# Kernel tuning notes

Measured on AMD Instinct MI355X. Metric: run time of the kernel, lower is better.

The kernel has to match this reference:

```python
import jax, jax.numpy as jnp
import numpy as np

D_X, D_K, D_V = 1024, 128, 128
B, N = 8, 2048


def setup_inputs() -> dict:
    key = jax.random.key(0)
    ks = jax.random.split(key, 7)
    s = lambda fan_in: 1.0 / np.sqrt(fan_in)
    return {
        "x": jax.random.normal(ks[0], (B, N, D_X), dtype=jnp.float32),
        "w_q": jax.random.uniform(ks[1], (D_K, D_X), jnp.float32, -s(D_X), s(D_X)),
        "b_q": jax.random.uniform(ks[2], (D_K,), jnp.float32, -s(D_X), s(D_X)),
        "w_k": jax.random.uniform(ks[3], (D_K, D_X), jnp.float32, -s(D_X), s(D_X)),
        "b_k": jax.random.uniform(ks[4], (D_K,), jnp.float32, -s(D_X), s(D_X)),
        "w_v": jax.random.uniform(ks[5], (D_V, D_X), jnp.float32, -s(D_X), s(D_X)),
        "b_v": jax.random.uniform(ks[6], (D_V,), jnp.float32, -s(D_X), s(D_X)),
    }


def reference(x, w_q, b_q, w_k, b_k, w_v, b_v):
    # Q is computed in the original module but unused; omit (no effect on output).
    K = jnp.einsum('bnx,kx->bnk', x, w_k) + b_k  # [B,N,d_k]
    V = jnp.einsum('bnx,vx->bnv', x, w_v) + b_v  # [B,N,d_v]
    # logits = K @ V^T / sqrt(d_k)  -> [B,N,N]  (note: K vs V, not Q vs K)
    scale = 1.0 / np.sqrt(D_K).astype(np.float32)
    logits = jnp.einsum('bnk,bmk->bnm', K, V) * scale
    attn = jax.nn.softmax(logits, axis=-1)
    return jnp.einsum('bnm,bmv->bnv', attn, V)
```

## Files before the change

### kernel.cpp

```cpp
#include <hip/hip_runtime.h>
#include <hip/hip_bf16.h>


typedef short s16x8 __attribute__((ext_vector_type(8)));
typedef float f32x4 __attribute__((ext_vector_type(4)));
typedef unsigned short u16;

#define AS1 __attribute__((address_space(1)))
#define AS3 __attribute__((address_space(3)))

__device__ __forceinline__ void gld_lds16(const void* g, void* l) {
  __builtin_amdgcn_global_load_lds((const AS1 unsigned int*)g, (AS3 unsigned int*)l, 16, 0, 0);
}

__device__ __forceinline__ float bf2f(u16 u) {
  unsigned int v = ((unsigned int)u) << 16;
  return __builtin_bit_cast(float, v);
}
__device__ __forceinline__ u16 f2bf(float f) {
  unsigned int u = __builtin_bit_cast(unsigned int, f);
  u += 0x7fffu + ((u >> 16) & 1u);
  return (u16)(u >> 16);
}
__device__ __forceinline__ unsigned pack_bf2(float a, float b) {
  unsigned ua = __builtin_bit_cast(unsigned, a) + 0x8000u;
  unsigned ub = __builtin_bit_cast(unsigned, b) + 0x8000u;
  return __builtin_amdgcn_perm(ub, ua, 0x07060302u);
}

__global__ __launch_bounds__(256, 4) void wconv_kernel(
    const float* __restrict__ wk, const float* __restrict__ wv,
    u16* __restrict__ wbf)
{
  const int e = (blockIdx.x * 256 + threadIdx.x) * 8;
  const float* src = (e < 131072) ? (wk + e) : (wv + (e - 131072));
  float4 a = *(const float4*)src;
  float4 b = *(const float4*)(src + 4);
  union { unsigned u[4]; s16x8 v; } pk;
  pk.u[0] = pack_bf2(a.x, a.y); pk.u[1] = pack_bf2(a.z, a.w);
  pk.u[2] = pack_bf2(b.x, b.y); pk.u[3] = pack_bf2(b.z, b.w);
  *(s16x8*)(wbf + e) = pk.v;
}

__global__ __launch_bounds__(256, 2) void kv_gemm_kernel(
    const float* __restrict__ x, const u16* __restrict__ wbf,
    const float* __restrict__ bk, const float* __restrict__ bv,
    u16* __restrict__ Kout, u16* __restrict__ Vout, u16* __restrict__ VTout)
{
  __shared__ u16 sA[2][4 * 512];
  __shared__ u16 sB[2][32 * 512];

  const int tid  = threadIdx.x;
  const int wave = tid >> 6;
  const int lane = tid & 63;
  const int l16  = lane & 15;
  const int lq   = lane >> 4;
  const int row0 = blockIdx.x * 32;

  f32x4 acc[2][4];
  for (int i = 0; i < 2; ++i)
    for (int j = 0; j < 4; ++j) acc[i][j] = (f32x4){0.f, 0.f, 0.f, 0.f};

  const int kc = tid & 7, arow = tid >> 3;
  const float* aSrc = x + (size_t)(row0 + arow) * 1024 + kc * 8;
  const int aSlot = ((((arow >> 4) * 2 + (kc >> 2)) * 64) + (kc & 3) * 16 + (arow & 15)) * 8;

  const u16* bSrc[8];
  for (int i = 0; i < 8; ++i) {
    const int sl = wave + i * 4;
    bSrc[i] = wbf + (size_t)((sl >> 1) * 16 + l16) * 1024 + (sl & 1) * 32 + lq * 8;
  }

  float4 p0a = *(const float4*)(aSrc);
  float4 p0b = *(const float4*)(aSrc + 4);
  float4 p1a = *(const float4*)(aSrc + 64);
  float4 p1b = *(const float4*)(aSrc + 68);
  for (int i = 0; i < 8; ++i)
    gld_lds16(bSrc[i], &sB[0][(wave + i * 4) * 512]);

  for (int s = 0; s < 16; ++s) {
    const int buf = s & 1;
    {
      union { unsigned u[4]; s16x8 v; } pk;
      pk.u[0] = pack_bf2(p0a.x, p0a.y); pk.u[1] = pack_bf2(p0a.z, p0a.w);
      pk.u[2] = pack_bf2(p0b.x, p0b.y); pk.u[3] = pack_bf2(p0b.z, p0b.w);
      *(s16x8*)(&sA[buf][aSlot]) = pk.v;
    }
    __syncthreads();
    if (s + 1 < 16)
      for (int i = 0; i < 8; ++i)
        gld_lds16(bSrc[i] + (s + 1) * 64, &sB[buf ^ 1][(wave + i * 4) * 512]);
    p0a = p1a; p0b = p1b;
    if (s + 2 < 16) {
      p1a = *(const float4*)(aSrc + (s + 2) * 64);
      p1b = *(const float4*)(aSrc + (s + 2) * 64 + 4);
    }
    s16x8 af[2][2], bf[4][2];
    for (int rb = 0; rb < 2; ++rb)
      for (int ks = 0; ks < 2; ++ks)
        af[rb][ks] = *(const s16x8*)(&sA[buf][((rb * 2 + ks) * 64 + lane) * 8]);
    for (int cb = 0; cb < 4; ++cb)
      for (int ks = 0; ks < 2; ++ks)
        bf[cb][ks] = *(const s16x8*)(&sB[buf][(((wave * 4 + cb) * 2 + ks) * 64 + lane) * 8]);
    for (int rb = 0; rb < 2; ++rb)
      for (int cb = 0; cb < 4; ++cb)
        for (int ks = 0; ks < 2; ++ks)
          acc[rb][cb] = __builtin_amdgcn_mfma_f32_16x16x32_bf16(af[rb][ks], bf[cb][ks], acc[rb][cb], 0, 0, 0);
  }

  const int  colBase = wave * 64;
  const bool isV = (wave >= 2);
  u16* outN = isV ? Vout : Kout;
  float fbias[4];
  for (int cb = 0; cb < 4; ++cb) {
    const int col = colBase + cb * 16 + l16;
    fbias[cb] = isV ? bv[col - 128] : bk[col];
  }
  for (int rb = 0; rb < 2; ++rb) {
    const int grow0 = row0 + rb * 16 + lq * 4;
    for (int cb = 0; cb < 4; ++cb) {
      const int gcol = colBase + cb * 16 + l16;
      const int ocol = isV ? (gcol - 128) : gcol;
      union { u16 u[4]; unsigned long long ull; } pk;
      for (int r = 0; r < 4; ++r) {
        u16 h = f2bf(acc[rb][cb][r] + fbias[cb]);
        outN[(size_t)(grow0 + r) * 128 + ocol] = h;
        pk.u[r] = h;
      }
      if (isV) {
        const int bidx = grow0 >> 11;
        const int n    = grow0 & 2047;
        *(unsigned long long*)(VTout + (size_t)bidx * 128 * 2048 + (size_t)ocol * 2048 + n) = pk.ull;
      }
    }
  }
}

__global__ __launch_bounds__(256, 2) void flash_kernel(
    const u16* __restrict__ Kmat, const u16* __restrict__ Vmat,
    const u16* __restrict__ VT, float* __restrict__ out,
    float* __restrict__ Opart, float* __restrict__ lbuf)
{
  __shared__ u16 sV[2][16 * 512];
  __shared__ u16 sVT[2][16 * 512];
  __shared__ u16 sP[64 * 66];

  const int tid  = threadIdx.x;
  const int wave = tid >> 6;
  const int lane = tid & 63;
  const int l16  = lane & 15;
  const int lq   = lane >> 4;
  const int b    = blockIdx.y;
  const int q0   = blockIdx.x * 64;
  const int z    = blockIdx.z;
  const int ntiles = (2048 / gridDim.z) / 64;
  const int mstart = z * (2048 / gridDim.z);
  const float scale = 0.08838834764831845f;

  s16x8 kf[4];
  {
    const u16* Kb = Kmat + ((size_t)b * 2048 + q0 + wave * 16 + l16) * 128 + lq * 8;
    for (int ks = 0; ks < 4; ++ks) kf[ks] = *(const s16x8*)(Kb + ks * 32);
  }

  const u16* vSrc[4];  const u16* vtSrc[4];
  {
    const u16* Vb  = Vmat + (size_t)b * 2048 * 128;
    const u16* VTb = VT   + (size_t)b * 128 * 2048;
    for (int i = 0; i < 4; ++i) {
      const int sl = wave + i * 4;
      vSrc[i]  = Vb  + (size_t)((sl >> 2) * 16 + l16) * 128 + (sl & 3) * 32 + lq * 8;
      vtSrc[i] = VTb + (size_t)((sl >> 1) * 16 + l16) * 2048 + (sl & 1) * 32 + lq * 8;
    }
  }

  f32x4 oacc[8];
  for (int v = 0; v < 8; ++v) oacc[v] = (f32x4){0.f, 0.f, 0.f, 0.f};
  float lrow[4] = {0.f, 0.f, 0.f, 0.f};

  for (int i = 0; i < 4; ++i) {
    gld_lds16(vSrc[i] + (size_t)mstart * 128, &sV[0][(wave + i * 4) * 512]);
    gld_lds16(vtSrc[i] + mstart,              &sVT[0][(wave + i * 4) * 512]);
  }

  for (int mt = 0; mt < ntiles; ++mt) {
    const int buf = mt & 1;
    __syncthreads();
    if (mt + 1 < ntiles) {
      const int m1 = mstart + (mt + 1) * 64;
      for (int i = 0; i < 4; ++i) {
        gld_lds16(vSrc[i] + (size_t)m1 * 128, &sV[buf ^ 1][(wave + i * 4) * 512]);
        gld_lds16(vtSrc[i] + m1,              &sVT[buf ^ 1][(wave + i * 4) * 512]);
      }
    }

    f32x4 sacc[4];
    for (int t = 0; t < 4; ++t) sacc[t] = (f32x4){0.f, 0.f, 0.f, 0.f};
    for (int ks = 0; ks < 4; ++ks)
      for (int t = 0; t < 4; ++t)
        sacc[t] = __builtin_amdgcn_mfma_f32_16x16x32_bf16(
            kf[ks], *(const s16x8*)(&sV[buf][(t * 4 + ks) * 512 + lane * 8]), sacc[t], 0, 0, 0);

    for (int r = 0; r < 4; ++r) {
      const int prow = (wave * 16 + lq * 4 + r) * 66;
      float rs = 0.f;
      for (int t = 0; t < 4; ++t) {
        float p = __expf(sacc[t][r] * scale);
        u16 h = f2bf(p);
        sP[prow + t * 16 + l16] = h;
        rs += bf2f(h);
      }
      lrow[r] += rs;
    }

    for (int ksm = 0; ksm < 2; ++ksm) {
      s16x8 a = *(const s16x8*)(&sP[(wave * 16 + l16) * 66 + ksm * 32 + lq * 8]);
      for (int v = 0; v < 8; ++v)
        oacc[v] = __builtin_amdgcn_mfma_f32_16x16x32_bf16(
            a, *(const s16x8*)(&sVT[buf][(v * 2 + ksm) * 512 + lane * 8]), oacc[v], 0, 0, 0);
    }
  }

  for (int r = 0; r < 4; ++r) {
    lrow[r] += __shfl_xor(lrow[r], 1);
    lrow[r] += __shfl_xor(lrow[r], 2);
    lrow[r] += __shfl_xor(lrow[r], 4);
    lrow[r] += __shfl_xor(lrow[r], 8);
  }

  const size_t rowg = (size_t)b * 2048 + q0 + wave * 16;
  if (gridDim.z == 1) {
    for (int r = 0; r < 4; ++r) {
      const float inv = 1.f / lrow[r];
      for (int v = 0; v < 8; ++v)
        out[(rowg + lq * 4 + r) * 128 + v * 16 + l16] = oacc[v][r] * inv;
    }
  } else {
    float* Op = Opart + (size_t)z * 2097152;
    float* lp = lbuf + (size_t)z * 32768;
    for (int r = 0; r < 4; ++r)
      for (int v = 0; v < 8; ++v)
        Op[(rowg + lq * 4 + r) * 128 + v * 16 + l16] = oacc[v][r];
    if (l16 == 0)
      for (int r = 0; r < 4; ++r)
        lp[rowg + lq * 4 + r] = lrow[r];
  }
}

__global__ __launch_bounds__(256, 4) void combine_kernel(
    const float* __restrict__ Opart, const float* __restrict__ lbuf,
    float* __restrict__ out)
{
  const int idx = blockIdx.x * 256 + threadIdx.x;
  const int row = idx >> 5;
  const float4 o0 = ((const float4*)Opart)[idx];
  const float4 o1 = ((const float4*)(Opart + 2097152))[idx];
  const float inv = 1.f / (lbuf[row] + lbuf[32768 + row]);
  float4 o;
  o.x = (o0.x + o1.x) * inv;
  o.y = (o0.y + o1.y) * inv;
  o.z = (o0.z + o1.z) * inv;
  o.w = (o0.w + o1.w) * inv;
  ((float4*)out)[idx] = o;
}

extern "C" void kernel_launch(void* const* d_in, const int* in_sizes, int n_in,
                              void* d_out, int out_size, void* d_ws, size_t ws_size,
                              hipStream_t stream) {
  const float* x  = (const float*)d_in[0];
  const float* wk = (const float*)d_in[3];
  const float* bk = (const float*)d_in[4];
  const float* wv = (const float*)d_in[5];
  const float* bv = (const float*)d_in[6];

  u16* ws   = (u16*)d_ws;
  u16* wbf  = ws;
  u16* Kmat = ws + 262144;
  u16* Vmat = Kmat + (size_t)16384 * 128;
  u16* VTm  = Vmat + (size_t)16384 * 128;
  float* Opart = (float*)(VTm + (size_t)16384 * 128);
  float* lbuf  = Opart + 2 * 2097152;
  const bool split = ws_size >= (size_t)30200000;

  wconv_kernel<<<128, 256, 0, stream>>>(wk, wv, wbf);
  kv_gemm_kernel<<<512, 256, 0, stream>>>(x, wbf, bk, bv, Kmat, Vmat, VTm);
  if (split) {
    flash_kernel<<<dim3(32, 8, 2), 256, 0, stream>>>(Kmat, Vmat, VTm,
                                                     (float*)d_out, Opart, lbuf);
    combine_kernel<<<2048, 256, 0, stream>>>(Opart, lbuf, (float*)d_out);
  } else {
    flash_kernel<<<dim3(32, 8, 1), 256, 0, stream>>>(Kmat, Vmat, VTm,
                                                     (float*)d_out, Opart, lbuf);
  }
}
```

Before: 182.0 us.

## Load GEMM weights and V tiles directly into registers instead of LDS staging

```diff
diff --git a/kernel.cpp b/kernel.cpp
--- a/kernel.cpp
+++ b/kernel.cpp
@@ -5,13 +5,6 @@
 typedef short s16x8 __attribute__((ext_vector_type(8)));
 typedef float f32x4 __attribute__((ext_vector_type(4)));
 typedef unsigned short u16;
-
-#define AS1 __attribute__((address_space(1)))
-#define AS3 __attribute__((address_space(3)))
-
-__device__ __forceinline__ void gld_lds16(const void* g, void* l) {
-  __builtin_amdgcn_global_load_lds((const AS1 unsigned int*)g, (AS3 unsigned int*)l, 16, 0, 0);
-}
 
 __device__ __forceinline__ float bf2f(u16 u) {
   unsigned int v = ((unsigned int)u) << 16;
@@ -26,6 +19,9 @@
   unsigned ua = __builtin_bit_cast(unsigned, a) + 0x8000u;
   unsigned ub = __builtin_bit_cast(unsigned, b) + 0x8000u;
   return __builtin_amdgcn_perm(ub, ua, 0x07060302u);
+}
+__device__ __forceinline__ void lgkm_barrier() {
+  asm volatile("s_waitcnt lgkmcnt(0)\n\ts_barrier" ::: "memory");
 }
 
 __global__ __launch_bounds__(256, 4) void wconv_kernel(
@@ -48,7 +44,6 @@
     u16* __restrict__ Kout, u16* __restrict__ Vout, u16* __restrict__ VTout)
 {
   __shared__ u16 sA[2][4 * 512];
-  __shared__ u16 sB[2][32 * 512];
 
   const int tid  = threadIdx.x;
   const int wave = tid >> 6;
@@ -65,47 +60,61 @@
   const float* aSrc = x + (size_t)(row0 + arow) * 1024 + kc * 8;
   const int aSlot = ((((arow >> 4) * 2 + (kc >> 2)) * 64) + (kc & 3) * 16 + (arow & 15)) * 8;
 
-  const u16* bSrc[8];
-  for (int i = 0; i < 8; ++i) {
-    const int sl = wave + i * 4;
-    bSrc[i] = wbf + (size_t)((sl >> 1) * 16 + l16) * 1024 + (sl & 1) * 32 + lq * 8;
-  }
-
-  float4 p0a = *(const float4*)(aSrc);
-  float4 p0b = *(const float4*)(aSrc + 4);
-  float4 p1a = *(const float4*)(aSrc + 64);
-  float4 p1b = *(const float4*)(aSrc + 68);
-  for (int i = 0; i < 8; ++i)
-    gld_lds16(bSrc[i], &sB[0][(wave + i * 4) * 512]);
+  const u16* bBase = wbf + (size_t)(wave * 64 + l16) * 1024 + lq * 8;
+  s16x8 bcur[8], bnxt[8];
+
+  {
+    float4 a0 = *(const float4*)aSrc;
+    float4 a1 = *(const float4*)(aSrc + 4);
+    union { unsigned u[4]; s16x8 v; } pk;
+    pk.u[0] = pack_bf2(a0.x, a0.y); pk.u[1] = pack_bf2(a0.z, a0.w);
+    pk.u[2] = pack_bf2(a1.x, a1.y); pk.u[3] = pack_bf2(a1.z, a1.w);
+    *(s16x8*)(&sA[0][aSlot]) = pk.v;
+  }
+  float4 p0a = *(const float4*)(aSrc + 64);
+  float4 p0b = *(const float4*)(aSrc + 68);
+  float4 p1a, p1b;
+#pragma unroll
+  for (int f = 0; f < 8; ++f)
+    bcur[f] = *(const s16x8*)(bBase + (f >> 1) * 16384 + (f & 1) * 32);
+  lgkm_barrier();
 
   for (int s = 0; s < 16; ++s) {
     const int buf = s & 1;
-    {
+    s16x8 af[2][2];
+#pragma unroll
+    for (int rb = 0; rb < 2; ++rb)
+#pragma unroll
+      for (int ks = 0; ks < 2; ++ks)
+        af[rb][ks] = *(const s16x8*)(&sA[buf][((rb * 2 + ks) * 64 + lane) * 8]);
+    if (s + 1 < 16) {
+      const int koff = (s + 1) * 64;
+#pragma unroll
+      for (int f = 0; f < 8; ++f)
+        bnxt[f] = *(const s16x8*)(bBase + (f >> 1) * 16384 + (f & 1) * 32 + koff);
+    }
+    if (s + 2 < 16) {
+      p1a = *(const float4*)(aSrc + (s + 2) * 64);
+      p1b = *(const float4*)(aSrc + (s + 2) * 64 + 4);
+    }
+#pragma unroll
+    for (int rb = 0; rb < 2; ++rb)
+#pragma unroll
+      for (int cb = 0; cb < 4; ++cb)
+#pragma unroll
+        for (int ks = 0; ks < 2; ++ks)
+          acc[rb][cb] = __builtin_amdgcn_mfma_f32_16x16x32_bf16(
+              af[rb][ks], bcur[cb * 2 + ks], acc[rb][cb], 0, 0, 0);
+    if (s + 1 < 16) {
       union { unsigned u[4]; s16x8 v; } pk;
       pk.u[0] = pack_bf2(p0a.x, p0a.y); pk.u[1] = pack_bf2(p0a.z, p0a.w);
       pk.u[2] = pack_bf2(p0b.x, p0b.y); pk.u[3] = pack_bf2(p0b.z, p0b.w);
-      *(s16x8*)(&sA[buf][aSlot]) = pk.v;
-    }
-    __syncthreads();
-    if (s + 1 < 16)
-      for (int i = 0; i < 8; ++i)
-        gld_lds16(bSrc[i] + (s + 1) * 64, &sB[buf ^ 1][(wave + i * 4) * 512]);
-    p0a = p1a; p0b = p1b;
-    if (s + 2 < 16) {
-      p1a = *(const float4*)(aSrc + (s + 2) * 64);
-      p1b = *(const float4*)(aSrc + (s + 2) * 64 + 4);
-    }
-    s16x8 af[2][2], bf[4][2];
-    for (int rb = 0; rb < 2; ++rb)
-      for (int ks = 0; ks < 2; ++ks)
-        af[rb][ks] = *(const s16x8*)(&sA[buf][((rb * 2 + ks) * 64 + lane) * 8]);
-    for (int cb = 0; cb < 4; ++cb)
-      for (int ks = 0; ks < 2; ++ks)
-        bf[cb][ks] = *(const s16x8*)(&sB[buf][(((wave * 4 + cb) * 2 + ks) * 64 + lane) * 8]);
-    for (int rb = 0; rb < 2; ++rb)
-      for (int cb = 0; cb < 4; ++cb)
-        for (int ks = 0; ks < 2; ++ks)
-          acc[rb][cb] = __builtin_amdgcn_mfma_f32_16x16x32_bf16(af[rb][ks], bf[cb][ks], acc[rb][cb], 0, 0, 0);
+      *(s16x8*)(&sA[buf ^ 1][aSlot]) = pk.v;
+      p0a = p1a; p0b = p1b;
+#pragma unroll
+      for (int f = 0; f < 8; ++f) bcur[f] = bnxt[f];
+    }
+    lgkm_barrier();
   }
 
   const int  colBase = wave * 64;
@@ -141,8 +150,6 @@
     const u16* __restrict__ VT, float* __restrict__ out,
     float* __restrict__ Opart, float* __restrict__ lbuf)
 {
-  __shared__ u16 sV[2][16 * 512];
-  __shared__ u16 sVT[2][16 * 512];
   __shared__ u16 sP[64 * 66];
 
   const int tid  = threadIdx.x;
@@ -150,60 +157,55 @@
   const int lane = tid & 63;
   const int l16  = lane & 15;
   const int lq   = lane >> 4;
-  const int b    = blockIdx.y;
-  const int q0   = blockIdx.x * 64;
-  const int z    = blockIdx.z;
-  const int ntiles = (2048 / gridDim.z) / 64;
-  const int mstart = z * (2048 / gridDim.z);
+  const int b    = blockIdx.x & 7;
+  const int q0   = ((blockIdx.x >> 3) & 31) * 64;
+  const int z    = blockIdx.x >> 8;
+  const int mstart = z * 1024;
   const float scale = 0.08838834764831845f;
 
   s16x8 kf[4];
   {
     const u16* Kb = Kmat + ((size_t)b * 2048 + q0 + wave * 16 + l16) * 128 + lq * 8;
+#pragma unroll
     for (int ks = 0; ks < 4; ++ks) kf[ks] = *(const s16x8*)(Kb + ks * 32);
   }
-
-  const u16* vSrc[4];  const u16* vtSrc[4];
-  {
-    const u16* Vb  = Vmat + (size_t)b * 2048 * 128;
-    const u16* VTb = VT   + (size_t)b * 128 * 2048;
-    for (int i = 0; i < 4; ++i) {
-      const int sl = wave + i * 4;
-      vSrc[i]  = Vb  + (size_t)((sl >> 2) * 16 + l16) * 128 + (sl & 3) * 32 + lq * 8;
-      vtSrc[i] = VTb + (size_t)((sl >> 1) * 16 + l16) * 2048 + (sl & 1) * 32 + lq * 8;
-    }
-  }
+  const u16* vrow  = Vmat + (size_t)b * 2048 * 128 + l16 * 128 + lq * 8;
+  const u16* vtrow = VT   + (size_t)b * 128 * 2048 + l16 * 2048 + lq * 8;
 
   f32x4 oacc[8];
   for (int v = 0; v < 8; ++v) oacc[v] = (f32x4){0.f, 0.f, 0.f, 0.f};
   float lrow[4] = {0.f, 0.f, 0.f, 0.f};
 
-  for (int i = 0; i < 4; ++i) {
-    gld_lds16(vSrc[i] + (size_t)mstart * 128, &sV[0][(wave + i * 4) * 512]);
-    gld_lds16(vtSrc[i] + mstart,              &sVT[0][(wave + i * 4) * 512]);
-  }
-
-  for (int mt = 0; mt < ntiles; ++mt) {
-    const int buf = mt & 1;
-    __syncthreads();
-    if (mt + 1 < ntiles) {
-      const int m1 = mstart + (mt + 1) * 64;
-      for (int i = 0; i < 4; ++i) {
-        gld_lds16(vSrc[i] + (size_t)m1 * 128, &sV[buf ^ 1][(wave + i * 4) * 512]);
-        gld_lds16(vtSrc[i] + m1,              &sVT[buf ^ 1][(wave + i * 4) * 512]);
-      }
-    }
-
+#pragma unroll 2
+  for (int mt = 0; mt < 16; ++mt) {
+    const int m0 = mstart + mt * 64;
+
+    s16x8 vf[16];
+#pragma unroll
+    for (int t = 0; t < 4; ++t)
+#pragma unroll
+      for (int ks = 0; ks < 4; ++ks)
+        vf[t * 4 + ks] = *(const s16x8*)(vrow + (size_t)(m0 + t * 16) * 128 + ks * 32);
     f32x4 sacc[4];
     for (int t = 0; t < 4; ++t) sacc[t] = (f32x4){0.f, 0.f, 0.f, 0.f};
+#pragma unroll
     for (int ks = 0; ks < 4; ++ks)
+#pragma unroll
       for (int t = 0; t < 4; ++t)
-        sacc[t] = __builtin_amdgcn_mfma_f32_16x16x32_bf16(
-            kf[ks], *(const s16x8*)(&sV[buf][(t * 4 + ks) * 512 + lane * 8]), sacc[t], 0, 0, 0);
-
+        sacc[t] = __builtin_amdgcn_mfma_f32_16x16x32_bf16(kf[ks], vf[t * 4 + ks], sacc[t], 0, 0, 0);
+
+    s16x8 vtf[16];
+#pragma unroll
+    for (int vt = 0; vt < 8; ++vt)
+#pragma unroll
+      for (int ksm = 0; ksm < 2; ++ksm)
+        vtf[vt * 2 + ksm] = *(const s16x8*)(vtrow + (size_t)vt * 32768 + m0 + ksm * 32);
+
+#pragma unroll
     for (int r = 0; r < 4; ++r) {
       const int prow = (wave * 16 + lq * 4 + r) * 66;
       float rs = 0.f;
+#pragma unroll
       for (int t = 0; t < 4; ++t) {
         float p = __expf(sacc[t][r] * scale);
         u16 h = f2bf(p);
@@ -213,11 +215,12 @@
       lrow[r] += rs;
     }
 
+#pragma unroll
     for (int ksm = 0; ksm < 2; ++ksm) {
       s16x8 a = *(const s16x8*)(&sP[(wave * 16 + l16) * 66 + ksm * 32 + lq * 8]);
-      for (int v = 0; v < 8; ++v)
-        oacc[v] = __builtin_amdgcn_mfma_f32_16x16x32_bf16(
-            a, *(const s16x8*)(&sVT[buf][(v * 2 + ksm) * 512 + lane * 8]), oacc[v], 0, 0, 0);
+#pragma unroll
+      for (int vt = 0; vt < 8; ++vt)
+        oacc[vt] = __builtin_amdgcn_mfma_f32_16x16x32_bf16(a, vtf[vt * 2 + ksm], oacc[vt], 0, 0, 0);
     }
   }
 
@@ -229,22 +232,14 @@
   }
 
   const size_t rowg = (size_t)b * 2048 + q0 + wave * 16;
-  if (gridDim.z == 1) {
-    for (int r = 0; r < 4; ++r) {
-      const float inv = 1.f / lrow[r];
-      for (int v = 0; v < 8; ++v)
-        out[(rowg + lq * 4 + r) * 128 + v * 16 + l16] = oacc[v][r] * inv;
-    }
-  } else {
-    float* Op = Opart + (size_t)z * 2097152;
-    float* lp = lbuf + (size_t)z * 32768;
+  float* Op = Opart + (size_t)z * 2097152;
+  float* lp = lbuf + (size_t)z * 32768;
+  for (int r = 0; r < 4; ++r)
+    for (int v = 0; v < 8; ++v)
+      Op[(rowg + lq * 4 + r) * 128 + v * 16 + l16] = oacc[v][r];
+  if (l16 == 0)
     for (int r = 0; r < 4; ++r)
-      for (int v = 0; v < 8; ++v)
-        Op[(rowg + lq * 4 + r) * 128 + v * 16 + l16] = oacc[v][r];
-    if (l16 == 0)
-      for (int r = 0; r < 4; ++r)
-        lp[rowg + lq * 4 + r] = lrow[r];
-  }
+      lp[rowg + lq * 4 + r] = lrow[r];
 }
 
 __global__ __launch_bounds__(256, 4) void combine_kernel(
@@ -280,16 +275,9 @@
   u16* VTm  = Vmat + (size_t)16384 * 128;
   float* Opart = (float*)(VTm + (size_t)16384 * 128);
   float* lbuf  = Opart + 2 * 2097152;
-  const bool split = ws_size >= (size_t)30200000;
 
   wconv_kernel<<<128, 256, 0, stream>>>(wk, wv, wbf);
   kv_gemm_kernel<<<512, 256, 0, stream>>>(x, wbf, bk, bv, Kmat, Vmat, VTm);
-  if (split) {
-    flash_kernel<<<dim3(32, 8, 2), 256, 0, stream>>>(Kmat, Vmat, VTm,
-                                                     (float*)d_out, Opart, lbuf);
-    combine_kernel<<<2048, 256, 0, stream>>>(Opart, lbuf, (float*)d_out);
-  } else {
-    flash_kernel<<<dim3(32, 8, 1), 256, 0, stream>>>(Kmat, Vmat, VTm,
-                                                     (float*)d_out, Opart, lbuf);
-  }
-}
+  flash_kernel<<<512, 256, 0, stream>>>(Kmat, Vmat, VTm, (float*)d_out, Opart, lbuf);
+  combine_kernel<<<2048, 256, 0, stream>>>(Opart, lbuf, (float*)d_out);
+}
```

Result: slower. 260.6 us (+43.2%).
